# Performance work log

Hardware: AMD Instinct MI355X
Metric: run time of the kernel (lower is better)

The kernel has to match this reference:

```python
import jax, jax.numpy as jnp
from jax import lax
import numpy as np

B, N, C = 16, 4096, 81          # batch, rois, classes (incl. background)
VARIANCES = np.array([0.1, 0.1, 0.2, 0.2], dtype=np.float32)
MAX_TOTAL = 200                  # max_total_size (= per-class cap here)
K = 200                          # per-class candidates kept before NMS
SCORE_TH = 0.5
IOU_TH = 0.5                     # tf combined NMS default
EPS = 1e-8


def setup_inputs() -> dict:
    key = jax.random.key(0)
    k1, k2, k3, k4 = jax.random.split(key, 4)
    yx = jax.random.uniform(k1, (B, N, 2)) * 0.8
    hw = 0.05 + jax.random.uniform(k2, (B, N, 2)) * 0.15
    roi_bboxes = jnp.concatenate([yx, yx + hw], axis=-1)          # [B,N,4] y1x1y2x2 in [0,1]
    pred_deltas = jax.random.normal(k3, (B, N, C * 4)) * 0.5      # [B,N,C*4]
    logits = jax.random.normal(k4, (B, N, C)) * 3.0
    pred_label_probs = jax.nn.softmax(logits, axis=-1)            # [B,N,C]
    return {"roi_bboxes": roi_bboxes, "pred_deltas": pred_deltas,
            "pred_label_probs": pred_label_probs}


def delta_to_bbox(anchors, deltas):
    # anchors [...,4] y1,x1,y2,x2 ; deltas [...,4] dy,dx,dh,dw
    ah = anchors[..., 2] - anchors[..., 0]
    aw = anchors[..., 3] - anchors[..., 1]
    acy = anchors[..., 0] + 0.5 * ah
    acx = anchors[..., 1] + 0.5 * aw
    bh = jnp.exp(deltas[..., 2]) * ah
    bw = jnp.exp(deltas[..., 3]) * aw
    bcy = deltas[..., 0] * ah + acy
    bcx = deltas[..., 1] * aw + acx
    y1 = bcy - 0.5 * bh
    x1 = bcx - 0.5 * bw
    return jnp.stack([y1, x1, y1 + bh, x1 + bw], axis=-1)


def pairwise_iou(boxes):  # [K,4] -> [K,K]
    y1 = jnp.maximum(boxes[:, None, 0], boxes[None, :, 0])
    x1 = jnp.maximum(boxes[:, None, 1], boxes[None, :, 1])
    y2 = jnp.minimum(boxes[:, None, 2], boxes[None, :, 2])
    x2 = jnp.minimum(boxes[:, None, 3], boxes[None, :, 3])
    inter = jnp.maximum(y2 - y1, 0.0) * jnp.maximum(x2 - x1, 0.0)
    area = jnp.maximum(boxes[:, 2] - boxes[:, 0], 0.0) * jnp.maximum(boxes[:, 3] - boxes[:, 1], 0.0)
    union = area[:, None] + area[None, :] - inter
    return inter / (union + EPS)


def _nms_keep(boxes_k, scores_k):
    # boxes_k [K,4] sorted by score desc; greedy suppression mask
    ious = pairwise_iou(boxes_k)
    rng = jnp.arange(K)
    valid = scores_k > SCORE_TH

    def step(keep, i):
        sup = (ious[i] > IOU_TH) & (rng > i) & keep[i]
        return keep & ~sup, None

    keep, _ = lax.scan(step, valid, rng)
    return keep


def _per_class(boxes_c, scores_c):
    # boxes_c [N,4], scores_c [N] -> top-K candidates + NMS-kept scores
    sc, idx = lax.top_k(scores_c, K)
    bx = boxes_c[idx]                       # [K,4]
    keep = _nms_keep(bx, sc)
    return bx, jnp.where(keep, sc, 0.0)


def _per_image(boxes_b, scores_b):
    # boxes_b [N,C,4], scores_b [N,C]
    bx, sc = jax.vmap(_per_class, in_axes=(1, 1))(boxes_b, scores_b)  # [C,K,4],[C,K]
    top_sc, top_idx = lax.top_k(sc.reshape(-1), MAX_TOTAL)
    top_bx = bx.reshape(-1, 4)[top_idx]
    top_lbl = (top_idx // K).astype(jnp.float32)
    valid = top_sc > 0.0
    top_bx = jnp.clip(jnp.where(valid[:, None], top_bx, 0.0), 0.0, 1.0)  # clip_boxes=True
    return top_bx, jnp.where(valid, top_sc, 0.0), jnp.where(valid, top_lbl, 0.0)


def reference(roi_bboxes, pred_deltas, pred_label_probs):
    b, n, _ = roi_bboxes.shape
    c = pred_label_probs.shape[-1]
    deltas = pred_deltas.reshape(b, n, c, 4) * jnp.asarray(VARIANCES)
    pred_bboxes = delta_to_bbox(roi_bboxes[:, :, None, :], deltas)       # [B,N,C,4]
    bg = jnp.argmax(pred_label_probs, axis=-1) == 0                      # background mask
    scores = jnp.where(bg[..., None], 0.0, pred_label_probs)             # [B,N,C]
    final_bboxes, final_scores, final_labels = jax.vmap(_per_image)(pred_bboxes, scores)
    return final_bboxes, final_labels, final_scores
```

## Files before the change

kernel.cpp:

```cpp
#include <hip/hip_runtime.h>
#include <math.h>

#pragma clang fp contract(off)

constexpr int NB  = 16;
constexpr int NR  = 4096;
constexpr int NC  = 81;
constexpr int NCM1 = NC - 1;
constexpr int KK  = 200;
constexpr int CAP = 4096;
constexpr int ROWS_PER_BLK = 64;
constexpr int CHUNKS = NR / ROWS_PER_BLK;
constexpr int GRID = NB * NR / ROWS_PER_BLK;
constexpr int MAXC = 1024;
constexpr int TCHUNK = 256;
constexpr int NCHUNK = CAP / TCHUNK;
constexpr float SCORE_TH = 0.5f;
constexpr float IOU_TH   = 0.5f;
constexpr float EPSF     = 1e-8f;

struct SK { float s; int key; };

__device__ __forceinline__ void decode_box(const float4& a, const float4& d,
                                           float& y1, float& x1, float& y2, float& x2) {
    float ah  = a.z - a.x;
    float aw  = a.w - a.y;
    float acy = a.x + 0.5f * ah;
    float acx = a.y + 0.5f * aw;
    float dy = d.x * 0.1f, dx = d.y * 0.1f;
    float dh = d.z * 0.2f, dw = d.w * 0.2f;
    float bh  = expf(dh) * ah;
    float bw  = expf(dw) * aw;
    float bcy = dy * ah + acy;
    float bcx = dx * aw + acx;
    y1 = bcy - 0.5f * bh;
    x1 = bcx - 0.5f * bw;
    y2 = y1 + bh;
    x2 = x1 + bw;
}

__global__ void k_classify(const float* __restrict__ roi,
                           const float* __restrict__ deltas,
                           const float* __restrict__ probs,
                           int* __restrict__ blk_cnt,
                           int* __restrict__ scls,
                           float2* __restrict__ ssr,
                           float4* __restrict__ sbox) {
    __shared__ float lp[ROWS_PER_BLK * NC];
    __shared__ int wcnt[4], wbase[4];
    const int bid = blockIdx.x, tid = threadIdx.x;

    const float4* src = (const float4*)(probs + (size_t)bid * ROWS_PER_BLK * NC);
    float4* dst = (float4*)lp;
    for (int v = tid; v < ROWS_PER_BLK * NC / 4; v += 256) dst[v] = src[v];
    __syncthreads();

    int g = tid >> 2;
    int j = tid & 3;
    const float* row = lp + g * NC;
    float m = -1.0f;
    int am = 127;
    for (int c = j; c < NC; c += 4) {
        float v = row[c];
        if (v > m) { m = v; am = c; }
    }
    for (int mask = 1; mask <= 2; mask <<= 1) {
        float om = __shfl_xor(m, mask);
        int   oi = __shfl_xor(am, mask);
        if (om > m || (om == m && oi < am)) { m = om; am = oi; }
    }

    bool pred = (j == 0) && (am != 0) && (m > SCORE_TH);
    unsigned long long bal = __ballot(pred);
    int lane = tid & 63, w = tid >> 6;
    if (lane == 0) wcnt[w] = __popcll(bal);
    __syncthreads();
    if (tid == 0) {
        int run = 0;
        for (int i = 0; i < 4; ++i) { wbase[i] = run; run += wcnt[i]; }
        blk_cnt[bid] = run;
    }
    __syncthreads();

    if (pred) {
        int pos = wbase[w] + __popcll(bal & ((1ull << lane) - 1ull));
        int r = bid * ROWS_PER_BLK + g;
        float4 a = ((const float4*)roi)[r];
        float4 d = *(const float4*)(deltas + ((size_t)r * NC + am) * 4);
        float y1, x1, y2, x2;
        decode_box(a, d, y1, x1, y2, x2);
        int idx = bid * ROWS_PER_BLK + pos;
        scls[idx] = am;
        ssr[idx]  = make_float2(m, (float)(r & (NR - 1)));
        sbox[idx] = make_float4(y1, x1, y2, x2);
    }
}

__global__ void k_perclass(const int* __restrict__ blk_cnt,
                           const int* __restrict__ scls,
                           const float2* __restrict__ ssr,
                           const float4* __restrict__ sbox,
                           int* __restrict__ kcnt,
                           SK* __restrict__ sk_seg,
                           float4* __restrict__ fbox_seg) {
    __shared__ int ccnt[CHUNKS];
    __shared__ int lcnt;
    __shared__ float ls[MAXC], lroi[MAXC];
    __shared__ unsigned short lidx[MAXC];
    __shared__ float ss[KK], sy1[KK], sx1[KK], sy2[KK], sx2[KK], sar[KK];
    __shared__ unsigned long long sup[KK][4];
    __shared__ int skeep[KK];

    const int bid = blockIdx.x, tid = threadIdx.x;
    const int b = bid / NCM1, cm1 = bid % NCM1, c = cm1 + 1;

    if (tid < CHUNKS) ccnt[tid] = blk_cnt[b * CHUNKS + tid];
    if (tid == 0) lcnt = 0;
    __syncthreads();

    const int* sc = scls + (size_t)b * NR;
    const float2* sr = ssr + (size_t)b * NR;
    for (int sidx = tid; sidx < NR; sidx += 256) {
        int chunk = sidx >> 6, s = sidx & 63;
        if (s < ccnt[chunk] && sc[sidx] == c) {
            int p = atomicAdd(&lcnt, 1);
            if (p < MAXC) {
                float2 v = sr[sidx];
                ls[p] = v.x; lroi[p] = v.y; lidx[p] = (unsigned short)sidx;
            }
        }
    }
    __syncthreads();
    int Mc = lcnt < MAXC ? lcnt : MAXC;
    if (Mc == 0) {
        if (tid == 0) kcnt[bid] = 0;
        return;
    }

    for (int i = tid; i < Mc; i += 256) {
        float si = ls[i], ri = lroi[i];
        int rank = 0;
        for (int jj = 0; jj < Mc; ++jj) {
            float sj = ls[jj], rj = lroi[jj];
            rank += (int)((sj > si) | ((sj == si) & (rj < ri)));
        }
        if (rank < KK) {
            float4 bx = sbox[(size_t)b * NR + lidx[i]];
            ss[rank] = si;
            sy1[rank] = bx.x; sx1[rank] = bx.y; sy2[rank] = bx.z; sx2[rank] = bx.w;
            sar[rank] = fmaxf(bx.z - bx.x, 0.f) * fmaxf(bx.w - bx.y, 0.f);
        }
    }
    __syncthreads();

    int L = Mc < KK ? Mc : KK;

    for (int idx = tid; idx < L * 4; idx += 256) {
        int i = idx >> 2, w = idx & 3;
        int j0 = w * 64;
        unsigned long long bits = 0;
        int jend = j0 + 64 < L ? j0 + 64 : L;
        int jstart = j0 > i + 1 ? j0 : i + 1;
        if (jstart < jend) {
            float yi1 = sy1[i], xi1 = sx1[i], yi2 = sy2[i], xi2 = sx2[i], ai = sar[i];
            for (int j = jstart; j < jend; ++j) {
                float yy1 = fmaxf(yi1, sy1[j]), xx1 = fmaxf(xi1, sx1[j]);
                float yy2 = fminf(yi2, sy2[j]), xx2 = fminf(xi2, sx2[j]);
                float inter = fmaxf(yy2 - yy1, 0.f) * fmaxf(xx2 - xx1, 0.f);
                float uni = ai + sar[j] - inter;
                if (inter / (uni + EPSF) > IOU_TH) bits |= 1ull << (j - j0);
            }
        }
        sup[i][w] = bits;
    }
    __syncthreads();

    if (tid < 64) {
        int lane = tid;
        int kmask = 0;
        #pragma unroll
        for (int s = 0; s < 4; ++s) if (s * 64 + lane < L) kmask |= 1 << s;
        for (int i = 0; i < L; ++i) {
            int oi = i & 63, si = i >> 6;
            unsigned long long r0 = sup[i][0], r1 = sup[i][1];
            unsigned long long r2 = sup[i][2], r3 = sup[i][3];
            int keep_i = (__shfl(kmask, oi) >> si) & 1;
            if (keep_i) {
                int supb = (int)((r0 >> lane) & 1)
                         | ((int)((r1 >> lane) & 1) << 1)
                         | ((int)((r2 >> lane) & 1) << 2)
                         | ((int)((r3 >> lane) & 1) << 3);
                kmask &= ~supb;
            }
        }
        #pragma unroll
        for (int s = 0; s < 4; ++s) {
            int jj = s * 64 + lane;
            if (jj < L) skeep[jj] = (kmask >> s) & 1;
        }
    }
    __syncthreads();

    for (int i = tid; i < L; i += 256) {
        if (skeep[i]) {
            int pos = 0;
            for (int j = 0; j < i; ++j) pos += skeep[j];
            size_t segbase = (size_t)bid * KK;
            sk_seg[segbase + pos].s = ss[i];
            sk_seg[segbase + pos].key = c * KK + i;
            fbox_seg[segbase + i] = make_float4(sy1[i], sx1[i], sy2[i], sx2[i]);
        }
    }
    if (tid == 0) {
        int tot = 0;
        for (int i = 0; i < L; ++i) tot += skeep[i];
        kcnt[bid] = tot;
    }
}

__global__ void k_topk(const int* __restrict__ kcnt,
                       const SK* __restrict__ sk_seg,
                       const float4* __restrict__ fbox_seg,
                       float* __restrict__ out) {
    int b = blockIdx.x / NCHUNK, chunk = blockIdx.x % NCHUNK;
    const int tid = threadIdx.x;

    __shared__ int pfx[NCM1 + 1];
    __shared__ SK  sL[CAP];

    if (tid < NCM1) pfx[tid + 1] = kcnt[b * NCM1 + tid];
    if (tid == 0) pfx[0] = 0;
    __syncthreads();
    if (tid == 0) {
        int run = 0;
        for (int s = 1; s <= NCM1; ++s) { run += pfx[s]; pfx[s] = run; }
    }
    __syncthreads();
    int M = pfx[NCM1];

    float* obox = out + (size_t)b * KK * 4;
    float* olbl = out + (size_t)NB * KK * 4 + (size_t)b * KK;
    float* osc  = out + (size_t)NB * KK * 5 + (size_t)b * KK;

    if (chunk == 0) {
        int Mi = M < KK ? M : KK;
        for (int i = Mi + tid; i < KK; i += 256) {
            obox[i * 4 + 0] = 0.f; obox[i * 4 + 1] = 0.f;
            obox[i * 4 + 2] = 0.f; obox[i * 4 + 3] = 0.f;
            olbl[i] = 0.f; osc[i] = 0.f;
        }
    }
    if (chunk * TCHUNK >= M) return;

    for (int i = tid; i < M; i += 256) {
        int lo = 0, hi = NCM1 - 1;
        while (lo < hi) {
            int mid = (lo + hi + 1) >> 1;
            if (pfx[mid] <= i) lo = mid; else hi = mid - 1;
        }
        int k = i - pfx[lo];
        sL[i] = sk_seg[((size_t)b * NCM1 + lo) * KK + k];
    }
    __syncthreads();

    int e = chunk * TCHUNK + tid;
    if (e >= M) return;
    float se = sL[e].s; int ke = sL[e].key;
    int rank = 0;
    const float4* p4 = (const float4*)sL;
    int npair = M >> 1;
    #pragma unroll 4
    for (int p = 0; p < npair; ++p) {
        float4 v = p4[p];
        int k0 = __float_as_int(v.y), k1 = __float_as_int(v.w);
        rank += (int)((v.x > se) | ((v.x == se) & (k0 < ke)));
        rank += (int)((v.z > se) | ((v.z == se) & (k1 < ke)));
    }
    if (M & 1) {
        float sj = sL[M - 1].s; int kj = sL[M - 1].key;
        rank += (int)((sj > se) | ((sj == se) & (kj < ke)));
    }
    if (rank < KK) {
        int cm1 = ke / KK - 1, ipre = ke % KK;
        float4 bx = fbox_seg[((size_t)b * NCM1 + cm1) * KK + ipre];
        obox[rank * 4 + 0] = fminf(fmaxf(bx.x, 0.f), 1.f);
        obox[rank * 4 + 1] = fminf(fmaxf(bx.y, 0.f), 1.f);
        obox[rank * 4 + 2] = fminf(fmaxf(bx.z, 0.f), 1.f);
        obox[rank * 4 + 3] = fminf(fmaxf(bx.w, 0.f), 1.f);
        olbl[rank] = (float)(ke / KK);
        osc[rank]  = se;
    }
}

extern "C" void kernel_launch(void* const* d_in, const int* in_sizes, int n_in,
                              void* d_out, int out_size, void* d_ws, size_t ws_size,
                              hipStream_t stream) {
    const float* roi    = (const float*)d_in[0];
    const float* deltas = (const float*)d_in[1];
    const float* probs  = (const float*)d_in[2];
    float* out = (float*)d_out;

    char* base = (char*)d_ws;
    int*    blk_cnt  = (int*)base;
    int*    kcnt     = (int*)(base + 4096);
    int*    scls     = (int*)(base + 16384);
    float2* ssr      = (float2*)(base + 16384 + 262144);
    float4* sbox     = (float4*)(base + 16384 + 262144 + 524288);
    SK*     sk_seg   = (SK*)(base + 16384 + 262144 + 524288 + 1048576);
    float4* fbox_seg = (float4*)(base + 16384 + 262144 + 524288 + 1048576 + 2097152);

    k_classify<<<GRID, 256, 0, stream>>>(roi, deltas, probs, blk_cnt,
                                         scls, ssr, sbox);
    k_perclass<<<NB * NCM1, 256, 0, stream>>>(blk_cnt, scls, ssr, sbox,
                                              kcnt, sk_seg, fbox_seg);
    k_topk<<<NB * NCHUNK, 256, 0, stream>>>(kcnt, sk_seg, fbox_seg, out);
}
```

Measured before the change: 69.22 us.

## Fuse per-class NMS and top-k via last-block finisher with histogram pre-filter

Box decoding moves from the classify kernel into the per-class kernel, so it runs only for the up-to-200 candidates of each class instead of every foreground row, and the sbox intermediate buffer disappears. The separate top-k kernel is folded into the per-class kernel: an atomic per-image counter elects the last block to finish. That block builds a score histogram to find a threshold bucket, keeps only candidates above it, and ranks them in shared memory with an overflow spill to global. This removes one launch and most of the rank-comparison work, at the cost of serialising each image's final top-k onto a single block, plus threadfence and atomic synchronisation.

New measurement: 125.6 us. +81.4%, slower.

```diff
diff --git a/kernel.cpp b/kernel.cpp
--- a/kernel.cpp
+++ b/kernel.cpp
@@ -8,13 +8,12 @@
 constexpr int NC  = 81;
 constexpr int NCM1 = NC - 1;
 constexpr int KK  = 200;
-constexpr int CAP = 4096;
 constexpr int ROWS_PER_BLK = 64;
 constexpr int CHUNKS = NR / ROWS_PER_BLK;
 constexpr int GRID = NB * NR / ROWS_PER_BLK;
 constexpr int MAXC = 1024;
-constexpr int TCHUNK = 256;
-constexpr int NCHUNK = CAP / TCHUNK;
+constexpr int NBKT = 2048;
+constexpr int PCAP = 2560;
 constexpr float SCORE_TH = 0.5f;
 constexpr float IOU_TH   = 0.5f;
 constexpr float EPSF     = 1e-8f;
@@ -39,16 +38,21 @@
     x2 = x1 + bw;
 }
 
-__global__ void k_classify(const float* __restrict__ roi,
-                           const float* __restrict__ deltas,
-                           const float* __restrict__ probs,
+__device__ __forceinline__ int bucketOf(float s) {
+    int bk = (int)((__float_as_uint(s) - 0x3F000000u) >> 12);
+    return bk < 0 ? 0 : (bk > NBKT - 1 ? NBKT - 1 : bk);
+}
+
+__global__ void k_classify(const float* __restrict__ probs,
                            int* __restrict__ blk_cnt,
                            int* __restrict__ scls,
                            float2* __restrict__ ssr,
-                           float4* __restrict__ sbox) {
+                           int* __restrict__ img_done) {
     __shared__ float lp[ROWS_PER_BLK * NC];
     __shared__ int wcnt[4], wbase[4];
     const int bid = blockIdx.x, tid = threadIdx.x;
+
+    if (tid == 0 && bid < NB) img_done[bid] = 0;
 
     const float4* src = (const float4*)(probs + (size_t)bid * ROWS_PER_BLK * NC);
     float4* dst = (float4*)lp;
@@ -85,36 +89,46 @@
     if (pred) {
         int pos = wbase[w] + __popcll(bal & ((1ull << lane) - 1ull));
         int r = bid * ROWS_PER_BLK + g;
-        float4 a = ((const float4*)roi)[r];
-        float4 d = *(const float4*)(deltas + ((size_t)r * NC + am) * 4);
-        float y1, x1, y2, x2;
-        decode_box(a, d, y1, x1, y2, x2);
         int idx = bid * ROWS_PER_BLK + pos;
         scls[idx] = am;
         ssr[idx]  = make_float2(m, (float)(r & (NR - 1)));
-        sbox[idx] = make_float4(y1, x1, y2, x2);
-    }
-}
-
-__global__ void k_perclass(const int* __restrict__ blk_cnt,
-                           const int* __restrict__ scls,
-                           const float2* __restrict__ ssr,
-                           const float4* __restrict__ sbox,
-                           int* __restrict__ kcnt,
-                           SK* __restrict__ sk_seg,
-                           float4* __restrict__ fbox_seg) {
-    __shared__ int ccnt[CHUNKS];
-    __shared__ int lcnt;
-    __shared__ float ls[MAXC], lroi[MAXC];
-    __shared__ unsigned short lidx[MAXC];
-    __shared__ float ss[KK], sy1[KK], sx1[KK], sy2[KK], sx2[KK], sar[KK];
-    __shared__ unsigned long long sup[KK][4];
-    __shared__ int skeep[KK];
+    }
+}
+
+__global__ __launch_bounds__(256)
+void k_pcfin(const float* __restrict__ roi,
+             const float* __restrict__ deltas,
+             const int* __restrict__ blk_cnt,
+             const int* __restrict__ scls,
+             const float2* __restrict__ ssr,
+             int* __restrict__ kcnt,
+             SK* __restrict__ sk_seg,
+             float4* __restrict__ fbox_seg,
+             SK* __restrict__ spill,
+             int* __restrict__ img_done,
+             float* __restrict__ out) {
+    union SM {
+        struct {
+            int ccnt[CHUNKS];
+            float ls[MAXC], lroi[MAXC];
+            float ss[KK], sy1[KK], sx1[KK], sy2[KK], sx2[KK], sar[KK];
+            unsigned long long sup[KK][4];
+            int skeep[KK];
+        } p;
+        struct {
+            int hist[NBKT];
+            int csum[256];
+            SK  pl[PCAP];
+            int pfx[NCM1 + 1];
+        } t;
+    };
+    __shared__ SM sm;
+    __shared__ int lcnt, lastflag, tshared, pcnt;
 
     const int bid = blockIdx.x, tid = threadIdx.x;
     const int b = bid / NCM1, cm1 = bid % NCM1, c = cm1 + 1;
 
-    if (tid < CHUNKS) ccnt[tid] = blk_cnt[b * CHUNKS + tid];
+    if (tid < CHUNKS) sm.p.ccnt[tid] = blk_cnt[b * CHUNKS + tid];
     if (tid == 0) lcnt = 0;
     __syncthreads();
 
@@ -122,173 +136,222 @@
     const float2* sr = ssr + (size_t)b * NR;
     for (int sidx = tid; sidx < NR; sidx += 256) {
         int chunk = sidx >> 6, s = sidx & 63;
-        if (s < ccnt[chunk] && sc[sidx] == c) {
+        if (s < sm.p.ccnt[chunk] && sc[sidx] == c) {
             int p = atomicAdd(&lcnt, 1);
             if (p < MAXC) {
                 float2 v = sr[sidx];
-                ls[p] = v.x; lroi[p] = v.y; lidx[p] = (unsigned short)sidx;
+                sm.p.ls[p] = v.x; sm.p.lroi[p] = v.y;
             }
         }
     }
     __syncthreads();
     int Mc = lcnt < MAXC ? lcnt : MAXC;
-    if (Mc == 0) {
+    int L = Mc < KK ? Mc : KK;
+
+    if (Mc > 0) {
+        for (int i = tid; i < Mc; i += 256) {
+            float si = sm.p.ls[i], ri = sm.p.lroi[i];
+            int rank = 0;
+            for (int jj = 0; jj < Mc; ++jj) {
+                float sj = sm.p.ls[jj], rj = sm.p.lroi[jj];
+                rank += (int)((sj > si) | ((sj == si) & (rj < ri)));
+            }
+            if (rank < KK) {
+                int r = (int)ri;
+                float4 a = ((const float4*)roi)[(size_t)b * NR + r];
+                float4 d = *(const float4*)(deltas + (((size_t)b * NR + r) * NC + c) * 4);
+                float y1, x1, y2, x2;
+                decode_box(a, d, y1, x1, y2, x2);
+                sm.p.ss[rank] = si;
+                sm.p.sy1[rank] = y1; sm.p.sx1[rank] = x1;
+                sm.p.sy2[rank] = y2; sm.p.sx2[rank] = x2;
+                sm.p.sar[rank] = fmaxf(y2 - y1, 0.f) * fmaxf(x2 - x1, 0.f);
+            }
+        }
+        __syncthreads();
+
+        for (int idx = tid; idx < L * 4; idx += 256) {
+            int i = idx >> 2, w = idx & 3;
+            int j0 = w * 64;
+            unsigned long long bits = 0;
+            int jend = j0 + 64 < L ? j0 + 64 : L;
+            int jstart = j0 > i + 1 ? j0 : i + 1;
+            if (jstart < jend) {
+                float yi1 = sm.p.sy1[i], xi1 = sm.p.sx1[i];
+                float yi2 = sm.p.sy2[i], xi2 = sm.p.sx2[i], ai = sm.p.sar[i];
+                for (int j = jstart; j < jend; ++j) {
+                    float yy1 = fmaxf(yi1, sm.p.sy1[j]), xx1 = fmaxf(xi1, sm.p.sx1[j]);
+                    float yy2 = fminf(yi2, sm.p.sy2[j]), xx2 = fminf(xi2, sm.p.sx2[j]);
+                    float inter = fmaxf(yy2 - yy1, 0.f) * fmaxf(xx2 - xx1, 0.f);
+                    float uni = ai + sm.p.sar[j] - inter;
+                    if (inter / (uni + EPSF) > IOU_TH) bits |= 1ull << (j - j0);
+                }
+            }
+            sm.p.sup[i][w] = bits;
+        }
+        __syncthreads();
+
+        if (tid < 64) {
+            int lane = tid;
+            int kmask = 0;
+            #pragma unroll
+            for (int s = 0; s < 4; ++s) if (s * 64 + lane < L) kmask |= 1 << s;
+            for (int i = 0; i < L; ++i) {
+                int oi = i & 63, si = i >> 6;
+                unsigned long long r0 = sm.p.sup[i][0], r1 = sm.p.sup[i][1];
+                unsigned long long r2 = sm.p.sup[i][2], r3 = sm.p.sup[i][3];
+                int keep_i = (__shfl(kmask, oi) >> si) & 1;
+                if (keep_i) {
+                    int supb = (int)((r0 >> lane) & 1)
+                             | ((int)((r1 >> lane) & 1) << 1)
+                             | ((int)((r2 >> lane) & 1) << 2)
+                             | ((int)((r3 >> lane) & 1) << 3);
+                    kmask &= ~supb;
+                }
+            }
+            #pragma unroll
+            for (int s = 0; s < 4; ++s) {
+                int jj = s * 64 + lane;
+                if (jj < L) sm.p.skeep[jj] = (kmask >> s) & 1;
+            }
+        }
+        __syncthreads();
+
+        for (int i = tid; i < L; i += 256) {
+            if (sm.p.skeep[i]) {
+                int pos = 0;
+                for (int j = 0; j < i; ++j) pos += sm.p.skeep[j];
+                size_t sb = (size_t)bid * KK;
+                sk_seg[sb + pos].s = sm.p.ss[i];
+                sk_seg[sb + pos].key = c * KK + i;
+                fbox_seg[sb + i] = make_float4(sm.p.sy1[i], sm.p.sx1[i],
+                                               sm.p.sy2[i], sm.p.sx2[i]);
+            }
+        }
+        if (tid == 0) {
+            int tot = 0;
+            for (int i = 0; i < L; ++i) tot += sm.p.skeep[i];
+            kcnt[bid] = tot;
+        }
+    } else {
         if (tid == 0) kcnt[bid] = 0;
-        return;
-    }
-
-    for (int i = tid; i < Mc; i += 256) {
-        float si = ls[i], ri = lroi[i];
-        int rank = 0;
-        for (int jj = 0; jj < Mc; ++jj) {
-            float sj = ls[jj], rj = lroi[jj];
-            rank += (int)((sj > si) | ((sj == si) & (rj < ri)));
-        }
-        if (rank < KK) {
-            float4 bx = sbox[(size_t)b * NR + lidx[i]];
-            ss[rank] = si;
-            sy1[rank] = bx.x; sx1[rank] = bx.y; sy2[rank] = bx.z; sx2[rank] = bx.w;
-            sar[rank] = fmaxf(bx.z - bx.x, 0.f) * fmaxf(bx.w - bx.y, 0.f);
-        }
-    }
-    __syncthreads();
-
-    int L = Mc < KK ? Mc : KK;
-
-    for (int idx = tid; idx < L * 4; idx += 256) {
-        int i = idx >> 2, w = idx & 3;
-        int j0 = w * 64;
-        unsigned long long bits = 0;
-        int jend = j0 + 64 < L ? j0 + 64 : L;
-        int jstart = j0 > i + 1 ? j0 : i + 1;
-        if (jstart < jend) {
-            float yi1 = sy1[i], xi1 = sx1[i], yi2 = sy2[i], xi2 = sx2[i], ai = sar[i];
-            for (int j = jstart; j < jend; ++j) {
-                float yy1 = fmaxf(yi1, sy1[j]), xx1 = fmaxf(xi1, sx1[j]);
-                float yy2 = fminf(yi2, sy2[j]), xx2 = fminf(xi2, sx2[j]);
-                float inter = fmaxf(yy2 - yy1, 0.f) * fmaxf(xx2 - xx1, 0.f);
-                float uni = ai + sar[j] - inter;
-                if (inter / (uni + EPSF) > IOU_TH) bits |= 1ull << (j - j0);
-            }
-        }
-        sup[i][w] = bits;
-    }
-    __syncthreads();
-
-    if (tid < 64) {
-        int lane = tid;
-        int kmask = 0;
-        #pragma unroll
-        for (int s = 0; s < 4; ++s) if (s * 64 + lane < L) kmask |= 1 << s;
-        for (int i = 0; i < L; ++i) {
-            int oi = i & 63, si = i >> 6;
-            unsigned long long r0 = sup[i][0], r1 = sup[i][1];
-            unsigned long long r2 = sup[i][2], r3 = sup[i][3];
-            int keep_i = (__shfl(kmask, oi) >> si) & 1;
-            if (keep_i) {
-                int supb = (int)((r0 >> lane) & 1)
-                         | ((int)((r1 >> lane) & 1) << 1)
-                         | ((int)((r2 >> lane) & 1) << 2)
-                         | ((int)((r3 >> lane) & 1) << 3);
-                kmask &= ~supb;
-            }
-        }
-        #pragma unroll
-        for (int s = 0; s < 4; ++s) {
-            int jj = s * 64 + lane;
-            if (jj < L) skeep[jj] = (kmask >> s) & 1;
-        }
-    }
-    __syncthreads();
-
-    for (int i = tid; i < L; i += 256) {
-        if (skeep[i]) {
-            int pos = 0;
-            for (int j = 0; j < i; ++j) pos += skeep[j];
-            size_t segbase = (size_t)bid * KK;
-            sk_seg[segbase + pos].s = ss[i];
-            sk_seg[segbase + pos].key = c * KK + i;
-            fbox_seg[segbase + i] = make_float4(sy1[i], sx1[i], sy2[i], sx2[i]);
-        }
-    }
+    }
+    __syncthreads();
+
+    __threadfence();
     if (tid == 0) {
-        int tot = 0;
-        for (int i = 0; i < L; ++i) tot += skeep[i];
-        kcnt[bid] = tot;
-    }
-}
-
-__global__ void k_topk(const int* __restrict__ kcnt,
-                       const SK* __restrict__ sk_seg,
-                       const float4* __restrict__ fbox_seg,
-                       float* __restrict__ out) {
-    int b = blockIdx.x / NCHUNK, chunk = blockIdx.x % NCHUNK;
-    const int tid = threadIdx.x;
-
-    __shared__ int pfx[NCM1 + 1];
-    __shared__ SK  sL[CAP];
-
-    if (tid < NCM1) pfx[tid + 1] = kcnt[b * NCM1 + tid];
-    if (tid == 0) pfx[0] = 0;
-    __syncthreads();
+        int v = atomicAdd(&img_done[b], 1);
+        lastflag = (v == NCM1 - 1);
+    }
+    __syncthreads();
+    if (!lastflag) return;
+    __threadfence();
+
     if (tid == 0) {
         int run = 0;
-        for (int s = 1; s <= NCM1; ++s) { run += pfx[s]; pfx[s] = run; }
-    }
-    __syncthreads();
-    int M = pfx[NCM1];
-
-    float* obox = out + (size_t)b * KK * 4;
-    float* olbl = out + (size_t)NB * KK * 4 + (size_t)b * KK;
-    float* osc  = out + (size_t)NB * KK * 5 + (size_t)b * KK;
-
-    if (chunk == 0) {
-        int Mi = M < KK ? M : KK;
-        for (int i = Mi + tid; i < KK; i += 256) {
-            obox[i * 4 + 0] = 0.f; obox[i * 4 + 1] = 0.f;
-            obox[i * 4 + 2] = 0.f; obox[i * 4 + 3] = 0.f;
-            olbl[i] = 0.f; osc[i] = 0.f;
-        }
-    }
-    if (chunk * TCHUNK >= M) return;
+        for (int s = 0; s < NCM1; ++s) { sm.t.pfx[s] = run; run += kcnt[b * NCM1 + s]; }
+        sm.t.pfx[NCM1] = run;
+        pcnt = 0;
+    }
+    for (int i = tid; i < NBKT; i += 256) sm.t.hist[i] = 0;
+    __syncthreads();
+    const int M = sm.t.pfx[NCM1];
+    const int minKM = M < KK ? M : KK;
 
     for (int i = tid; i < M; i += 256) {
         int lo = 0, hi = NCM1 - 1;
         while (lo < hi) {
             int mid = (lo + hi + 1) >> 1;
-            if (pfx[mid] <= i) lo = mid; else hi = mid - 1;
-        }
-        int k = i - pfx[lo];
-        sL[i] = sk_seg[((size_t)b * NCM1 + lo) * KK + k];
-    }
-    __syncthreads();
-
-    int e = chunk * TCHUNK + tid;
-    if (e >= M) return;
-    float se = sL[e].s; int ke = sL[e].key;
-    int rank = 0;
-    const float4* p4 = (const float4*)sL;
-    int npair = M >> 1;
-    #pragma unroll 4
-    for (int p = 0; p < npair; ++p) {
-        float4 v = p4[p];
-        int k0 = __float_as_int(v.y), k1 = __float_as_int(v.w);
-        rank += (int)((v.x > se) | ((v.x == se) & (k0 < ke)));
-        rank += (int)((v.z > se) | ((v.z == se) & (k1 < ke)));
-    }
-    if (M & 1) {
-        float sj = sL[M - 1].s; int kj = sL[M - 1].key;
-        rank += (int)((sj > se) | ((sj == se) & (kj < ke)));
-    }
-    if (rank < KK) {
-        int cm1 = ke / KK - 1, ipre = ke % KK;
-        float4 bx = fbox_seg[((size_t)b * NCM1 + cm1) * KK + ipre];
-        obox[rank * 4 + 0] = fminf(fmaxf(bx.x, 0.f), 1.f);
-        obox[rank * 4 + 1] = fminf(fmaxf(bx.y, 0.f), 1.f);
-        obox[rank * 4 + 2] = fminf(fmaxf(bx.z, 0.f), 1.f);
-        obox[rank * 4 + 3] = fminf(fmaxf(bx.w, 0.f), 1.f);
-        olbl[rank] = (float)(ke / KK);
-        osc[rank]  = se;
+            if (sm.t.pfx[mid] <= i) lo = mid; else hi = mid - 1;
+        }
+        SK v = sk_seg[((size_t)b * NCM1 + lo) * KK + (i - sm.t.pfx[lo])];
+        atomicAdd(&sm.t.hist[bucketOf(v.s)], 1);
+    }
+    __syncthreads();
+
+    {
+        int s8 = 0;
+        #pragma unroll
+        for (int k = 0; k < NBKT / 256; ++k) s8 += sm.t.hist[tid * (NBKT / 256) + k];
+        sm.t.csum[tid] = s8;
+    }
+    __syncthreads();
+    if (tid == 0) {
+        int cum = 0, tb = 0;
+        for (int ch = 255; ch >= 0; --ch) {
+            if (cum + sm.t.csum[ch] >= minKM) {
+                for (int bk = ch * (NBKT / 256) + (NBKT / 256) - 1; bk >= ch * (NBKT / 256); --bk) {
+                    cum += sm.t.hist[bk];
+                    if (cum >= minKM) { tb = bk; break; }
+                }
+                break;
+            }
+            cum += sm.t.csum[ch];
+        }
+        tshared = tb;
+    }
+    __syncthreads();
+    const int tb = tshared;
+
+    SK* spill_b = spill + (size_t)b * NR;
+    for (int i = tid; i < M; i += 256) {
+        int lo = 0, hi = NCM1 - 1;
+        while (lo < hi) {
+            int mid = (lo + hi + 1) >> 1;
+            if (sm.t.pfx[mid] <= i) lo = mid; else hi = mid - 1;
+        }
+        SK v = sk_seg[((size_t)b * NCM1 + lo) * KK + (i - sm.t.pfx[lo])];
+        if (bucketOf(v.s) >= tb) {
+            int pos = atomicAdd(&pcnt, 1);
+            if (pos < PCAP) sm.t.pl[pos] = v;
+            else            spill_b[pos] = v;
+        }
+    }
+    __syncthreads();
+    const int P = pcnt;
+    const int PL = P < PCAP ? P : PCAP;
+
+    float* obox = out + (size_t)b * KK * 4;
+    float* olbl = out + (size_t)NB * KK * 4 + (size_t)b * KK;
+    float* osc  = out + (size_t)NB * KK * 5 + (size_t)b * KK;
+
+    for (int i = minKM + tid; i < KK; i += 256) {
+        obox[i * 4 + 0] = 0.f; obox[i * 4 + 1] = 0.f;
+        obox[i * 4 + 2] = 0.f; obox[i * 4 + 3] = 0.f;
+        olbl[i] = 0.f; osc[i] = 0.f;
+    }
+
+    const float4* p4 = (const float4*)sm.t.pl;
+    const int npair = PL >> 1;
+    for (int ti = tid; ti < P; ti += 256) {
+        SK me = (ti < PCAP) ? sm.t.pl[ti] : spill_b[ti];
+        float se = me.s; int ke = me.key;
+        int rank = 0;
+        #pragma unroll 4
+        for (int p = 0; p < npair; ++p) {
+            float4 v = p4[p];
+            int k0 = __float_as_int(v.y), k1 = __float_as_int(v.w);
+            rank += (int)((v.x > se) | ((v.x == se) & (k0 < ke)));
+            rank += (int)((v.z > se) | ((v.z == se) & (k1 < ke)));
+        }
+        if (PL & 1) {
+            SK v = sm.t.pl[PL - 1];
+            rank += (int)((v.s > se) | ((v.s == se) & (v.key < ke)));
+        }
+        for (int j = PCAP; j < P; ++j) {
+            SK v = spill_b[j];
+            rank += (int)((v.s > se) | ((v.s == se) & (v.key < ke)));
+        }
+        if (rank < KK) {
+            int scm1 = ke / KK - 1, ipre = ke % KK;
+            float4 bx = fbox_seg[((size_t)b * NCM1 + scm1) * KK + ipre];
+            obox[rank * 4 + 0] = fminf(fmaxf(bx.x, 0.f), 1.f);
+            obox[rank * 4 + 1] = fminf(fmaxf(bx.y, 0.f), 1.f);
+            obox[rank * 4 + 2] = fminf(fmaxf(bx.z, 0.f), 1.f);
+            obox[rank * 4 + 3] = fminf(fmaxf(bx.w, 0.f), 1.f);
+            olbl[rank] = (float)(ke / KK);
+            osc[rank]  = se;
+        }
     }
 }
 
@@ -301,17 +364,17 @@
     float* out = (float*)d_out;
 
     char* base = (char*)d_ws;
-    int*    blk_cnt  = (int*)base;
-    int*    kcnt     = (int*)(base + 4096);
+    int*    blk_cnt  = (int*)(base);
+    int*    img_done = (int*)(base + 8192);
     int*    scls     = (int*)(base + 16384);
-    float2* ssr      = (float2*)(base + 16384 + 262144);
-    float4* sbox     = (float4*)(base + 16384 + 262144 + 524288);
-    SK*     sk_seg   = (SK*)(base + 16384 + 262144 + 524288 + 1048576);
-    float4* fbox_seg = (float4*)(base + 16384 + 262144 + 524288 + 1048576 + 2097152);
-
-    k_classify<<<GRID, 256, 0, stream>>>(roi, deltas, probs, blk_cnt,
-                                         scls, ssr, sbox);
-    k_perclass<<<NB * NCM1, 256, 0, stream>>>(blk_cnt, scls, ssr, sbox,
-                                              kcnt, sk_seg, fbox_seg);
-    k_topk<<<NB * NCHUNK, 256, 0, stream>>>(kcnt, sk_seg, fbox_seg, out);
-}
+    float2* ssr      = (float2*)(base + 278528);
+    int*    kcnt     = (int*)(base + 802816);
+    SK*     sk_seg   = (SK*)(base + 811008);
+    float4* fbox_seg = (float4*)(base + 2908160);
+    SK*     spill    = (SK*)(base + 7102464);
+
+    k_classify<<<GRID, 256, 0, stream>>>(probs, blk_cnt, scls, ssr, img_done);
+    k_pcfin<<<NB * NCM1, 256, 0, stream>>>(roi, deltas, blk_cnt, scls, ssr,
+                                           kcnt, sk_seg, fbox_seg, spill,
+                                           img_done, out);
+}
```
